# Optimization experiments

Hardware: AMD Instinct MI355X
Metric: run time of the kernel (lower is better)

The kernel has to match this reference:

```python
import jax, jax.numpy as jnp
import numpy as np

N = 50000
E = 800000
IN_C = 128
HID = 8
OUT_C = 32
HEADS = (4, 4, 4)
NEG_SLOPE = 0.2


def gat_conv(x, src, dst, W, att_src, att_dst, bias, heads, out_c, concat):
    # x: [N, F_in]; W: [F_in, heads*out_c]; att_*: [heads, out_c]; bias: [heads*out_c] or [out_c]
    n = x.shape[0]
    h = (x @ W).reshape(n, heads, out_c)                      # [N, H, C]
    a_src = (h * att_src).sum(-1)                             # [N, H]
    a_dst = (h * att_dst).sum(-1)                             # [N, H]
    e = jax.nn.leaky_relu(a_src[src] + a_dst[dst], NEG_SLOPE)  # [E, H]
    # segment softmax over edges grouped by destination node
    m = jax.ops.segment_max(e, dst, num_segments=n)           # [N, H]
    m = jnp.where(jnp.isfinite(m), m, 0.0)
    p = jnp.exp(e - m[dst])                                   # [E, H]
    s = jax.ops.segment_sum(p, dst, num_segments=n)           # [N, H]
    alpha = p / (s[dst] + 1e-16)                              # [E, H]
    msg = h[src] * alpha[:, :, None]                          # [E, H, C]
    out = jax.ops.segment_sum(msg, dst, num_segments=n)       # [N, H, C]
    out = out.reshape(n, heads * out_c) if concat else out.mean(axis=1)
    return out + bias


def setup_inputs() -> dict:
    key = jax.random.key(0)
    ks = jax.random.split(key, 16)
    x = jax.random.normal(ks[0], (N, IN_C), dtype=jnp.float32)
    edge_index = jax.random.randint(ks[1], (2, E), 0, N, dtype=jnp.int64)
    c1 = HID                       # per-head out of conv1 (8)
    c2 = HID * HEADS[0]            # per-head out of conv2 (32)
    c3 = OUT_C                     # per-head out of conv3 (32)
    in2 = HID * HEADS[0]           # 32
    in3 = HID * HEADS[0] * HEADS[1]  # 128
    sc = 0.1
    return {
        "x": x,
        "edge_index": edge_index,
        "W1": jax.random.normal(ks[2], (IN_C, HEADS[0] * c1), dtype=jnp.float32) * sc,
        "as1": jax.random.normal(ks[3], (HEADS[0], c1), dtype=jnp.float32) * sc,
        "ad1": jax.random.normal(ks[4], (HEADS[0], c1), dtype=jnp.float32) * sc,
        "b1": jnp.zeros((HEADS[0] * c1,), dtype=jnp.float32),
        "W2": jax.random.normal(ks[5], (in2, HEADS[1] * c2), dtype=jnp.float32) * sc,
        "as2": jax.random.normal(ks[6], (HEADS[1], c2), dtype=jnp.float32) * sc,
        "ad2": jax.random.normal(ks[7], (HEADS[1], c2), dtype=jnp.float32) * sc,
        "b2": jnp.zeros((HEADS[1] * c2,), dtype=jnp.float32),
        "W3": jax.random.normal(ks[8], (in3, HEADS[2] * c3), dtype=jnp.float32) * sc,
        "as3": jax.random.normal(ks[9], (HEADS[2], c3), dtype=jnp.float32) * sc,
        "ad3": jax.random.normal(ks[10], (HEADS[2], c3), dtype=jnp.float32) * sc,
        "b3": jnp.zeros((c3,), dtype=jnp.float32),
    }


def reference(x, edge_index, W1, as1, ad1, b1, W2, as2, ad2, b2, W3, as3, ad3, b3):
    src, dst = edge_index[0], edge_index[1]
    h = gat_conv(x, src, dst, W1, as1, ad1, b1, HEADS[0], HID, True)
    h = jax.nn.elu(h)
    h = gat_conv(h, src, dst, W2, as2, ad2, b2, HEADS[1], HID * HEADS[0], True)
    h = jax.nn.elu(h)
    out = gat_conv(h, src, dst, W3, as3, ad3, b3, HEADS[2], OUT_C, False)
    return out
```

## Files before the change

### kernel.cpp

```cpp
#include <hip/hip_runtime.h>
#include <hip/hip_fp16.h>

#define NEG_SLOPE 0.2f

static inline int cdiv(long long a, long long b) { return (int)((a + b - 1) / b); }

typedef _Float16 f16x8 __attribute__((ext_vector_type(8)));
typedef float f32x4 __attribute__((ext_vector_type(4)));

union h4u {
    float2  f2;
    __half2 h2[2];
};

__device__ __forceinline__ void load_sd(const void* ei_raw, int is64, int e, int E_,
                                        int& s, int& d)
{
    if (is64) {
        const long long* p = (const long long*)ei_raw;
        s = (int)p[e];
        d = (int)p[E_ + e];
    } else {
        const int* p = (const int*)ei_raw;
        s = p[e];
        d = p[E_ + e];
    }
}

__global__ __launch_bounds__(256) void prep_kernel(
    const void* __restrict__ ei, int E_, int n, int* __restrict__ flag,
    int* __restrict__ deg,
    const float* __restrict__ W1, __half* __restrict__ Wt1,
    const float* __restrict__ W2, __half* __restrict__ Wt2,
    const float* __restrict__ W3, __half* __restrict__ Wt3)
{
    int idx = blockIdx.x * 256 + threadIdx.x;

    if (blockIdx.x == 0) {
        __shared__ int bad;
        if (threadIdx.x == 0) bad = 0;
        __syncthreads();
        const long long* e64 = (const long long*)ei;
        int cnt = E_ < 512 ? E_ : 512;
        bool ok = true;
        for (int i = threadIdx.x; i < cnt; i += 256) {
            long long v = e64[i];
            if (v < 0 || v >= n) ok = false;
        }
        if (!ok) atomicAdd(&bad, 1);
        __syncthreads();
        if (threadIdx.x == 0) *flag = (bad == 0) ? 1 : 0;
    }

    if (idx < n) deg[idx] = 0;

    if (idx < 128 * 32) {
        int k = idx / 32, c = idx % 32;
        Wt1[c * 128 + k] = __float2half(W1[idx]);
    }
    if (idx < 32 * 128) {
        int k = idx / 128, c = idx % 128;
        Wt2[c * 32 + k] = __float2half(W2[idx]);
    }
    if (idx < 128 * 128) {
        int k = idx / 128, c = idx % 128;
        Wt3[c * 128 + k] = __float2half(W3[idx]);
    }
}

__global__ __launch_bounds__(256) void hist_kernel(const void* __restrict__ ei_raw,
                                                   const int* __restrict__ flag,
                                                   int* __restrict__ deg,
                                                   unsigned short* __restrict__ s16,
                                                   unsigned short* __restrict__ d16,
                                                   unsigned short* __restrict__ r16,
                                                   int E_)
{
    int base = blockIdx.x * 1024 + threadIdx.x;
    int is64 = *flag;
    int sj[4], dj[4], rj[4];
    bool v[4];
#pragma unroll
    for (int j = 0; j < 4; j++) {
        int e = base + j * 256;
        v[j] = e < E_;
        if (v[j]) load_sd(ei_raw, is64, e, E_, sj[j], dj[j]);
    }
#pragma unroll
    for (int j = 0; j < 4; j++) {
        int e = base + j * 256;
        if (v[j]) {
            s16[e] = (unsigned short)sj[j];
            d16[e] = (unsigned short)dj[j];
        }
    }
#pragma unroll
    for (int j = 0; j < 4; j++) {
        if (v[j]) rj[j] = atomicAdd(deg + dj[j], 1);
    }
#pragma unroll
    for (int j = 0; j < 4; j++) {
        int e = base + j * 256;
        if (v[j]) r16[e] = (unsigned short)rj[j];
    }
}

__device__ __forceinline__ int wave_incl_scan(int v)
{
    int lane = threadIdx.x & 63;
#pragma unroll
    for (int off = 1; off < 64; off <<= 1) {
        int t = __shfl_up(v, off);
        if (lane >= off) v += t;
    }
    return v;
}

__global__ __launch_bounds__(1024) void scan_part_kernel(const int* __restrict__ deg,
                                                         int* __restrict__ start,
                                                         int* __restrict__ bsum, int n)
{
    __shared__ int wsum[16];
    int i = blockIdx.x * 1024 + threadIdx.x;
    int wid = threadIdx.x >> 6, lane = threadIdx.x & 63;
    int v = (i < n) ? deg[i] : 0;
    int incl = wave_incl_scan(v);
    if (lane == 63) wsum[wid] = incl;
    __syncthreads();
    if (wid == 0) {
        int w = (lane < 16) ? wsum[lane] : 0;
        w = wave_incl_scan(w);
        if (lane < 16) wsum[lane] = w;
    }
    __syncthreads();
    int excl = incl - v + (wid ? wsum[wid - 1] : 0);
    if (i < n) start[i] = excl;
    if (threadIdx.x == 1023) bsum[blockIdx.x] = wsum[15];
}

__global__ __launch_bounds__(1024) void scan_add_kernel(const int* __restrict__ deg,
                                                        const int* __restrict__ bsum,
                                                        int* __restrict__ start, int n)
{
    __shared__ int off_sh;
    if (threadIdx.x == 0) {
        int s = 0;
        for (int j = 0; j < blockIdx.x; j++) s += bsum[j];
        off_sh = s;
    }
    __syncthreads();
    int i = blockIdx.x * 1024 + threadIdx.x;
    if (i >= n) return;
    int v = start[i] + off_sh;
    start[i] = v;
    if (i == n - 1) start[n] = v + deg[i];
}

__global__ __launch_bounds__(256) void scatter_kernel(
    const unsigned short* __restrict__ s16, const unsigned short* __restrict__ d16,
    const unsigned short* __restrict__ r16, const int* __restrict__ start,
    unsigned short* __restrict__ sorted_src, int E_)
{
    int base = blockIdx.x * 1024 + threadIdx.x;
    int sj[4], dj[4], rj[4];
    bool v[4];
#pragma unroll
    for (int j = 0; j < 4; j++) {
        int e = base + j * 256;
        v[j] = e < E_;
        sj[j] = v[j] ? (int)s16[e] : 0;
        dj[j] = v[j] ? (int)d16[e] : 0;
        rj[j] = v[j] ? (int)r16[e] : 0;
    }
    int pj[4];
#pragma unroll
    for (int j = 0; j < 4; j++) {
        if (v[j]) pj[j] = start[dj[j]] + rj[j];
    }
#pragma unroll
    for (int j = 0; j < 4; j++) {
        if (v[j])
            __builtin_nontemporal_store((unsigned short)sj[j], sorted_src + pj[j]);
    }
}

template <int K, int NOUT, int A16>
__global__ __launch_bounds__(256) void gemm_mfma_kernel(
    const void* __restrict__ xin, const __half* __restrict__ Wt,
    const float* __restrict__ att_s, const float* __restrict__ att_d,
    __half* __restrict__ h, float* __restrict__ a_s, float* __restrict__ a_d, int n)
{
    constexpr int KC = 32;
    constexpr int NT = NOUT / 16;
    constexpr int XP = KC + 8;
    constexpr int HP = NOUT + 8;
    constexpr int C  = NOUT / 4;

    __shared__ _Float16 Xs[64 * XP];
    __shared__ _Float16 Ws[NOUT * XP];
    __shared__ _Float16 Hs[64 * HP];
    __shared__ float As[NOUT], Ad[NOUT];

    const int tid  = threadIdx.x;
    const int nb   = blockIdx.x * 64;
    const int wave = tid >> 6, lane = tid & 63;
    const int m16  = lane & 15, quad = lane >> 4;

    if (tid < NOUT) { As[tid] = att_s[tid]; Ad[tid] = att_d[tid]; }

    f32x4 acc[NT];
#pragma unroll
    for (int t = 0; t < NT; t++) acc[t] = (f32x4){0.f, 0.f, 0.f, 0.f};

    for (int kc = 0; kc < K; kc += KC) {
        {
            int node = tid >> 2, seg = tid & 3;
            int gn = nb + node;
            f16x8 v = {0, 0, 0, 0, 0, 0, 0, 0};
            if (gn < n) {
                if (A16) {
                    v = *(const f16x8*)((const __half*)xin + (size_t)gn * K + kc +
                                        seg * 8);
                } else {
                    const float4* p =
                        (const float4*)((const float*)xin + (size_t)gn * K + kc + seg * 8);
                    float4 a = p[0], b = p[1];
                    v = (f16x8){(_Float16)a.x, (_Float16)a.y, (_Float16)a.z,
                                (_Float16)a.w, (_Float16)b.x, (_Float16)b.y,
                                (_Float16)b.z, (_Float16)b.w};
                }
            }
            *(f16x8*)&Xs[node * XP + seg * 8] = v;
        }
        for (int u = tid; u < NOUT * 4; u += 256) {
            int col = u >> 2, seg = u & 3;
            *(f16x8*)&Ws[col * XP + seg * 8] =
                *(const f16x8*)(Wt + (size_t)col * K + kc + seg * 8);
        }
        __syncthreads();

        f16x8 a = *(const f16x8*)&Xs[(wave * 16 + m16) * XP + quad * 8];
#pragma unroll
        for (int t = 0; t < NT; t++) {
            f16x8 b = *(const f16x8*)&Ws[(t * 16 + m16) * XP + quad * 8];
            acc[t] = __builtin_amdgcn_mfma_f32_16x16x32_f16(a, b, acc[t], 0, 0, 0);
        }
        __syncthreads();
    }

#pragma unroll
    for (int t = 0; t < NT; t++) {
#pragma unroll
        for (int r = 0; r < 4; r++) {
            int row = wave * 16 + quad * 4 + r;
            Hs[row * HP + t * 16 + m16] = (_Float16)acc[t][r];
        }
    }
    __syncthreads();

    for (int u = tid; u < 64 * NOUT / 8; u += 256) {
        int row = u / (NOUT / 8), seg = u % (NOUT / 8);
        int gn = nb + row;
        if (gn < n)
            *(f16x8*)(h + (size_t)gn * NOUT + seg * 8) =
                *(const f16x8*)&Hs[row * HP + seg * 8];
    }

    {
        int node = tid >> 2, head = tid & 3;
        int gn = nb + node;
        const _Float16* hr = &Hs[node * HP + head * C];
        float s1 = 0.f, s2 = 0.f;
#pragma unroll 4
        for (int c = 0; c < C; c++) {
            float v = (float)hr[c];
            s1 += v * As[head * C + c];
            s2 += v * Ad[head * C + c];
        }
        if (gn < n) {
            a_s[gn * 4 + head] = s1;
            a_d[gn * 4 + head] = s2;
        }
    }
}

template <int MODE>
__global__ __launch_bounds__(256) void gat_agg128_kernel(
    const int* __restrict__ start, const unsigned short* __restrict__ ss,
    const __half* __restrict__ h, const float* __restrict__ a_s,
    const float* __restrict__ a_d, const float* __restrict__ bias,
    void* __restrict__ out, int n)
{
    int local = threadIdx.x >> 5;
    int q     = threadIdx.x & 31;
    int node  = blockIdx.x * 8 + local;
    bool active = node < n;
    int s0 = 0, s1 = 0;
    if (active) { s0 = start[node]; s1 = start[node + 1]; }
    int head = q >> 3;
    float adh = active ? a_d[node * 4 + head] : 0.f;
    const float2* __restrict__ h2 = (const float2*)h + q;

    float4 acc = make_float4(0.f, 0.f, 0.f, 0.f);
    float sm = 0.f;
    int i = s0;
    for (; i + 8 <= s1; i += 8) {
        int    sj[8];
        float  ej[8];
        float2 rj[8];
#pragma unroll
        for (int j = 0; j < 8; j++) sj[j] = (int)ss[i + j];
#pragma unroll
        for (int j = 0; j < 8; j++) ej[j] = a_s[sj[j] * 4 + head];
#pragma unroll
        for (int j = 0; j < 8; j++) rj[j] = h2[(size_t)sj[j] * 32];
#pragma unroll
        for (int j = 0; j < 8; j++) {
            float e = ej[j] + adh;
            e = e > 0.f ? e : NEG_SLOPE * e;
            float p = __expf(e);
            sm += p;
            h4u u; u.f2 = rj[j];
            float2 lo = __half22float2(u.h2[0]);
            float2 hi = __half22float2(u.h2[1]);
            acc.x += lo.x * p; acc.y += lo.y * p;
            acc.z += hi.x * p; acc.w += hi.y * p;
        }
    }
    for (; i < s1; i++) {
        int s = (int)ss[i];
        float e = a_s[s * 4 + head] + adh;
        e = e > 0.f ? e : NEG_SLOPE * e;
        float p = __expf(e);
        sm += p;
        h4u u; u.f2 = h2[(size_t)s * 32];
        float2 lo = __half22float2(u.h2[0]);
        float2 hi = __half22float2(u.h2[1]);
        acc.x += lo.x * p; acc.y += lo.y * p;
        acc.z += hi.x * p; acc.w += hi.y * p;
    }

    float inv = 1.f / (sm + 1e-16f);
    acc.x *= inv; acc.y *= inv; acc.z *= inv; acc.w *= inv;

    if (MODE == 0) {
        if (active) {
            float4 b4 = ((const float4*)bias)[q];
            float4 v = make_float4(acc.x + b4.x, acc.y + b4.y, acc.z + b4.z,
                                   acc.w + b4.w);
            v.x = v.x > 0.f ? v.x : (__expf(v.x) - 1.f);
            v.y = v.y > 0.f ? v.y : (__expf(v.y) - 1.f);
            v.z = v.z > 0.f ? v.z : (__expf(v.z) - 1.f);
            v.w = v.w > 0.f ? v.w : (__expf(v.w) - 1.f);
            h4u u;
            u.h2[0] = __floats2half2_rn(v.x, v.y);
            u.h2[1] = __floats2half2_rn(v.z, v.w);
            *(float2*)((__half*)out + (size_t)node * 128 + q * 4) = u.f2;
        }
    } else {
        __shared__ float4 sh4[8][33];
        sh4[local][q] = acc;
        __syncthreads();
        if (q < 8 && active) {
            float4 a = sh4[local][q];
            float4 b = sh4[local][q + 8];
            float4 c = sh4[local][q + 16];
            float4 d = sh4[local][q + 24];
            float4 b4 = ((const float4*)bias)[q];
            float4 r = make_float4(0.25f * (a.x + b.x + c.x + d.x) + b4.x,
                                   0.25f * (a.y + b.y + c.y + d.y) + b4.y,
                                   0.25f * (a.z + b.z + c.z + d.z) + b4.z,
                                   0.25f * (a.w + b.w + c.w + d.w) + b4.w);
            *(float4*)((float*)out + (size_t)node * 32 + q * 4) = r;
        }
    }
}

__global__ __launch_bounds__(256) void gat_agg32_kernel(
    const int* __restrict__ start, const unsigned short* __restrict__ ss,
    const __half* __restrict__ h, const float* __restrict__ a_s,
    const float* __restrict__ a_d, const float* __restrict__ bias,
    __half* __restrict__ out, int n)
{
    int local = threadIdx.x >> 3;
    int q     = threadIdx.x & 7;
    int node  = blockIdx.x * 32 + local;
    bool active = node < n;
    int s0 = 0, s1 = 0;
    if (active) { s0 = start[node]; s1 = start[node + 1]; }
    int head = q >> 1;
    float adh = active ? a_d[node * 4 + head] : 0.f;
    const float2* __restrict__ h2 = (const float2*)h + q;

    float4 acc = make_float4(0.f, 0.f, 0.f, 0.f);
    float sm = 0.f;
    int i = s0;
    for (; i + 8 <= s1; i += 8) {
        int    sj[8];
        float  ej[8];
        float2 rj[8];
#pragma unroll
        for (int j = 0; j < 8; j++) sj[j] = (int)ss[i + j];
#pragma unroll
        for (int j = 0; j < 8; j++) ej[j] = a_s[sj[j] * 4 + head];
#pragma unroll
        for (int j = 0; j < 8; j++) rj[j] = h2[(size_t)sj[j] * 8];
#pragma unroll
        for (int j = 0; j < 8; j++) {
            float e = ej[j] + adh;
            e = e > 0.f ? e : NEG_SLOPE * e;
            float p = __expf(e);
            sm += p;
            h4u u; u.f2 = rj[j];
            float2 lo = __half22float2(u.h2[0]);
            float2 hi = __half22float2(u.h2[1]);
            acc.x += lo.x * p; acc.y += lo.y * p;
            acc.z += hi.x * p; acc.w += hi.y * p;
        }
    }
    for (; i < s1; i++) {
        int s = (int)ss[i];
        float e = a_s[s * 4 + head] + adh;
        e = e > 0.f ? e : NEG_SLOPE * e;
        float p = __expf(e);
        sm += p;
        h4u u; u.f2 = h2[(size_t)s * 8];
        float2 lo = __half22float2(u.h2[0]);
        float2 hi = __half22float2(u.h2[1]);
        acc.x += lo.x * p; acc.y += lo.y * p;
        acc.z += hi.x * p; acc.w += hi.y * p;
    }

    if (active) {
        float inv = 1.f / (sm + 1e-16f);
        float4 b4 = ((const float4*)bias)[q];
        float4 v = make_float4(acc.x * inv + b4.x, acc.y * inv + b4.y,
                               acc.z * inv + b4.z, acc.w * inv + b4.w);
        v.x = v.x > 0.f ? v.x : (__expf(v.x) - 1.f);
        v.y = v.y > 0.f ? v.y : (__expf(v.y) - 1.f);
        v.z = v.z > 0.f ? v.z : (__expf(v.z) - 1.f);
        v.w = v.w > 0.f ? v.w : (__expf(v.w) - 1.f);
        h4u u;
        u.h2[0] = __floats2half2_rn(v.x, v.y);
        u.h2[1] = __floats2half2_rn(v.z, v.w);
        *(float2*)(out + (size_t)node * 32 + q * 4) = u.f2;
    }
}


extern "C" void kernel_launch(void* const* d_in, const int* in_sizes, int n_in,
                              void* d_out, int out_size, void* d_ws, size_t ws_size,
                              hipStream_t stream)
{
    const float* x   = (const float*)d_in[0];
    const void*  ei  = d_in[1];
    const float* W1  = (const float*)d_in[2];
    const float* as1 = (const float*)d_in[3];
    const float* ad1 = (const float*)d_in[4];
    const float* b1  = (const float*)d_in[5];
    const float* W2  = (const float*)d_in[6];
    const float* as2 = (const float*)d_in[7];
    const float* ad2 = (const float*)d_in[8];
    const float* b2  = (const float*)d_in[9];
    const float* W3  = (const float*)d_in[10];
    const float* as3 = (const float*)d_in[11];
    const float* ad3 = (const float*)d_in[12];
    const float* b3  = (const float*)d_in[13];
    float* out = (float*)d_out;

    const int N_ = in_sizes[0] / 128;
    const int E_ = in_sizes[1] / 2;

    char* ws = (char*)d_ws;
    size_t off = 0;
    auto alloc = [&](size_t nbytes) -> void* {
        void* p = ws + off;
        off += (nbytes + 255) & ~(size_t)255;
        return p;
    };
    __half* h          = (__half*)alloc((size_t)N_ * 128 * 2);
    __half* x2h        = (__half*)alloc((size_t)N_ * 32 * 2);
    __half* x3h        = (__half*)alloc((size_t)N_ * 128 * 2);
    __half* Wt1        = (__half*)alloc(128 * 32 * 2);
    __half* Wt2        = (__half*)alloc(32 * 128 * 2);
    __half* Wt3        = (__half*)alloc(128 * 128 * 2);
    float* asrc        = (float*)alloc((size_t)N_ * 4 * 4);
    float* adst        = (float*)alloc((size_t)N_ * 4 * 4);
    int*   deg         = (int*)alloc((size_t)N_ * 4);
    int*   start       = (int*)alloc((size_t)(N_ + 1) * 4);
    unsigned short* sorted_src = (unsigned short*)alloc((size_t)E_ * 2);
    unsigned short* s16        = (unsigned short*)alloc((size_t)E_ * 2);
    unsigned short* d16        = (unsigned short*)alloc((size_t)E_ * 2);
    unsigned short* r16        = (unsigned short*)alloc((size_t)E_ * 2);
    int*   bsum        = (int*)alloc(4096);
    int*   flag        = (int*)alloc(256);

    const int gN8  = cdiv(N_, 8);
    const int gN32 = cdiv(N_, 32);
    const int gN64 = cdiv(N_, 64);
    const int nSB  = cdiv(N_, 1024);
    int prepWork = N_ > 128 * 128 ? N_ : 128 * 128;

    prep_kernel<<<cdiv(prepWork, 256), 256, 0, stream>>>(ei, E_, N_, flag, deg,
                                                         W1, Wt1, W2, Wt2, W3, Wt3);
    hist_kernel<<<cdiv(E_, 1024), 256, 0, stream>>>(ei, flag, deg, s16, d16, r16, E_);
    scan_part_kernel<<<nSB, 1024, 0, stream>>>(deg, start, bsum, N_);
    scan_add_kernel<<<nSB, 1024, 0, stream>>>(deg, bsum, start, N_);
    scatter_kernel<<<cdiv(E_, 1024), 256, 0, stream>>>(s16, d16, r16, start,
                                                       sorted_src, E_);

    gemm_mfma_kernel<128, 32, 0><<<gN64, 256, 0, stream>>>(x, Wt1, as1, ad1, h,
                                                           asrc, adst, N_);
    gat_agg32_kernel<<<gN32, 256, 0, stream>>>(start, sorted_src, h, asrc, adst, b1,
                                               x2h, N_);

    gemm_mfma_kernel<32, 128, 1><<<gN64, 256, 0, stream>>>(x2h, Wt2, as2, ad2, h,
                                                           asrc, adst, N_);
    gat_agg128_kernel<0><<<gN8, 256, 0, stream>>>(start, sorted_src, h, asrc, adst, b2,
                                                  x3h, N_);

    gemm_mfma_kernel<128, 128, 1><<<gN64, 256, 0, stream>>>(x3h, Wt3, as3, ad3, h,
                                                            asrc, adst, N_);
    gat_agg128_kernel<1><<<gN8, 256, 0, stream>>>(start, sorted_src, h, asrc, adst, b3,
                                                  out, N_);
}
```

Measured before the change: 285.9 us.

## Fuse CSR build into one cooperative kernel and deepen aggregation unroll

```diff
diff --git a/kernel.cpp b/kernel.cpp
--- a/kernel.cpp
+++ b/kernel.cpp
@@ -1,5 +1,8 @@
 #include <hip/hip_runtime.h>
 #include <hip/hip_fp16.h>
+#include <hip/hip_cooperative_groups.h>
+
+namespace cg = cooperative_groups;
 
 #define NEG_SLOPE 0.2f
 
@@ -27,19 +30,51 @@
     }
 }
 
-__global__ __launch_bounds__(256) void prep_kernel(
-    const void* __restrict__ ei, int E_, int n, int* __restrict__ flag,
+__device__ __forceinline__ int wave_incl_scan(int v)
+{
+    int lane = threadIdx.x & 63;
+#pragma unroll
+    for (int off = 1; off < 64; off <<= 1) {
+        int t = __shfl_up(v, off);
+        if (lane >= off) v += t;
+    }
+    return v;
+}
+
+__global__ __launch_bounds__(256) void csr_kernel(
+    const void* __restrict__ ei, int E_, int n,
     int* __restrict__ deg,
+    unsigned short* __restrict__ s16, unsigned short* __restrict__ d16,
+    unsigned short* __restrict__ r16,
+    int* __restrict__ start, int* __restrict__ bsum,
+    unsigned short* __restrict__ sorted_src,
     const float* __restrict__ W1, __half* __restrict__ Wt1,
     const float* __restrict__ W2, __half* __restrict__ Wt2,
     const float* __restrict__ W3, __half* __restrict__ Wt3)
 {
-    int idx = blockIdx.x * 256 + threadIdx.x;
-
-    if (blockIdx.x == 0) {
-        __shared__ int bad;
-        if (threadIdx.x == 0) bad = 0;
-        __syncthreads();
+    cg::grid_group grid = cg::this_grid();
+    const int nB    = gridDim.x;
+    const int gsize = nB * 256;
+    const int gtid  = blockIdx.x * 256 + threadIdx.x;
+
+    for (int i = gtid; i < n; i += gsize) deg[i] = 0;
+    for (int i = gtid; i < 128 * 32; i += gsize) {
+        int k = i / 32, c = i % 32;
+        Wt1[c * 128 + k] = __float2half(W1[i]);
+    }
+    for (int i = gtid; i < 32 * 128; i += gsize) {
+        int k = i / 128, c = i % 128;
+        Wt2[c * 32 + k] = __float2half(W2[i]);
+    }
+    for (int i = gtid; i < 128 * 128; i += gsize) {
+        int k = i / 128, c = i % 128;
+        Wt3[c * 128 + k] = __float2half(W3[i]);
+    }
+
+    __shared__ int bad_sh;
+    if (threadIdx.x == 0) bad_sh = 0;
+    __syncthreads();
+    {
         const long long* e64 = (const long long*)ei;
         int cnt = E_ < 512 ? E_ : 512;
         bool ok = true;
@@ -47,140 +82,108 @@
             long long v = e64[i];
             if (v < 0 || v >= n) ok = false;
         }
-        if (!ok) atomicAdd(&bad, 1);
-        __syncthreads();
-        if (threadIdx.x == 0) *flag = (bad == 0) ? 1 : 0;
-    }
-
-    if (idx < n) deg[idx] = 0;
-
-    if (idx < 128 * 32) {
-        int k = idx / 32, c = idx % 32;
-        Wt1[c * 128 + k] = __float2half(W1[idx]);
-    }
-    if (idx < 32 * 128) {
-        int k = idx / 128, c = idx % 128;
-        Wt2[c * 32 + k] = __float2half(W2[idx]);
-    }
-    if (idx < 128 * 128) {
-        int k = idx / 128, c = idx % 128;
-        Wt3[c * 128 + k] = __float2half(W3[idx]);
-    }
-}
-
-__global__ __launch_bounds__(256) void hist_kernel(const void* __restrict__ ei_raw,
-                                                   const int* __restrict__ flag,
-                                                   int* __restrict__ deg,
-                                                   unsigned short* __restrict__ s16,
-                                                   unsigned short* __restrict__ d16,
-                                                   unsigned short* __restrict__ r16,
-                                                   int E_)
-{
-    int base = blockIdx.x * 1024 + threadIdx.x;
-    int is64 = *flag;
-    int sj[4], dj[4], rj[4];
-    bool v[4];
-#pragma unroll
-    for (int j = 0; j < 4; j++) {
-        int e = base + j * 256;
-        v[j] = e < E_;
-        if (v[j]) load_sd(ei_raw, is64, e, E_, sj[j], dj[j]);
-    }
-#pragma unroll
-    for (int j = 0; j < 4; j++) {
-        int e = base + j * 256;
-        if (v[j]) {
-            s16[e] = (unsigned short)sj[j];
-            d16[e] = (unsigned short)dj[j];
-        }
-    }
-#pragma unroll
-    for (int j = 0; j < 4; j++) {
-        if (v[j]) rj[j] = atomicAdd(deg + dj[j], 1);
-    }
-#pragma unroll
-    for (int j = 0; j < 4; j++) {
-        int e = base + j * 256;
-        if (v[j]) r16[e] = (unsigned short)rj[j];
-    }
-}
-
-__device__ __forceinline__ int wave_incl_scan(int v)
-{
-    int lane = threadIdx.x & 63;
-#pragma unroll
-    for (int off = 1; off < 64; off <<= 1) {
-        int t = __shfl_up(v, off);
-        if (lane >= off) v += t;
-    }
-    return v;
-}
-
-__global__ __launch_bounds__(1024) void scan_part_kernel(const int* __restrict__ deg,
-                                                         int* __restrict__ start,
-                                                         int* __restrict__ bsum, int n)
-{
-    __shared__ int wsum[16];
-    int i = blockIdx.x * 1024 + threadIdx.x;
-    int wid = threadIdx.x >> 6, lane = threadIdx.x & 63;
-    int v = (i < n) ? deg[i] : 0;
-    int incl = wave_incl_scan(v);
-    if (lane == 63) wsum[wid] = incl;
+        if (!ok) atomicAdd(&bad_sh, 1);
+    }
     __syncthreads();
-    if (wid == 0) {
-        int w = (lane < 16) ? wsum[lane] : 0;
-        w = wave_incl_scan(w);
-        if (lane < 16) wsum[lane] = w;
-    }
+    const int is64 = (bad_sh == 0);
+
+    grid.sync();
+
+    for (int base = blockIdx.x * 1024 + threadIdx.x; base < E_; base += gsize * 4) {
+        int sj[4], dj[4], rj[4];
+        bool v[4];
+#pragma unroll
+        for (int j = 0; j < 4; j++) {
+            int e = base + j * 256;
+            v[j] = e < E_;
+            if (v[j]) load_sd(ei, is64, e, E_, sj[j], dj[j]);
+        }
+#pragma unroll
+        for (int j = 0; j < 4; j++) {
+            int e = base + j * 256;
+            if (v[j]) {
+                s16[e] = (unsigned short)sj[j];
+                d16[e] = (unsigned short)dj[j];
+            }
+        }
+#pragma unroll
+        for (int j = 0; j < 4; j++) {
+            if (v[j]) rj[j] = atomicAdd(deg + dj[j], 1);
+        }
+#pragma unroll
+        for (int j = 0; j < 4; j++) {
+            int e = base + j * 256;
+            if (v[j]) r16[e] = (unsigned short)rj[j];
+        }
+    }
+
+    grid.sync();
+
+    const int C  = (n + nB - 1) / nB;
+    const int c0 = blockIdx.x * C;
+    const int c1 = (c0 + C) < n ? (c0 + C) : n;
+    __shared__ int wsum[4];
+    __shared__ int carry_sh;
+    if (threadIdx.x == 0) carry_sh = 0;
     __syncthreads();
-    int excl = incl - v + (wid ? wsum[wid - 1] : 0);
-    if (i < n) start[i] = excl;
-    if (threadIdx.x == 1023) bsum[blockIdx.x] = wsum[15];
-}
-
-__global__ __launch_bounds__(1024) void scan_add_kernel(const int* __restrict__ deg,
-                                                        const int* __restrict__ bsum,
-                                                        int* __restrict__ start, int n)
-{
-    __shared__ int off_sh;
-    if (threadIdx.x == 0) {
-        int s = 0;
-        for (int j = 0; j < blockIdx.x; j++) s += bsum[j];
-        off_sh = s;
-    }
-    __syncthreads();
-    int i = blockIdx.x * 1024 + threadIdx.x;
-    if (i >= n) return;
-    int v = start[i] + off_sh;
-    start[i] = v;
-    if (i == n - 1) start[n] = v + deg[i];
-}
-
-__global__ __launch_bounds__(256) void scatter_kernel(
-    const unsigned short* __restrict__ s16, const unsigned short* __restrict__ d16,
-    const unsigned short* __restrict__ r16, const int* __restrict__ start,
-    unsigned short* __restrict__ sorted_src, int E_)
-{
-    int base = blockIdx.x * 1024 + threadIdx.x;
-    int sj[4], dj[4], rj[4];
-    bool v[4];
-#pragma unroll
-    for (int j = 0; j < 4; j++) {
-        int e = base + j * 256;
-        v[j] = e < E_;
-        sj[j] = v[j] ? (int)s16[e] : 0;
-        dj[j] = v[j] ? (int)d16[e] : 0;
-        rj[j] = v[j] ? (int)r16[e] : 0;
-    }
-    int pj[4];
-#pragma unroll
-    for (int j = 0; j < 4; j++) {
-        if (v[j]) pj[j] = start[dj[j]] + rj[j];
-    }
-#pragma unroll
-    for (int j = 0; j < 4; j++) {
-        if (v[j])
-            __builtin_nontemporal_store((unsigned short)sj[j], sorted_src + pj[j]);
+    for (int t = c0; t < c1; t += 256) {
+        int i = t + threadIdx.x;
+        int v = (i < c1) ? deg[i] : 0;
+        int incl = wave_incl_scan(v);
+        int wid = threadIdx.x >> 6, lane = threadIdx.x & 63;
+        if (lane == 63) wsum[wid] = incl;
+        __syncthreads();
+        int woff = 0;
+        for (int w = 0; w < wid; w++) woff += wsum[w];
+        int carry = carry_sh;
+        int excl = incl - v + woff + carry;
+        if (i < c1) start[i] = excl;
+        __syncthreads();
+        if (threadIdx.x == 255) carry_sh = carry + woff + incl;
+        __syncthreads();
+    }
+    if (threadIdx.x == 0) bsum[blockIdx.x] = carry_sh;
+
+    grid.sync();
+
+    __shared__ int red[256];
+    {
+        int partial = 0;
+        for (int j = threadIdx.x; j < blockIdx.x; j += 256) partial += bsum[j];
+        red[threadIdx.x] = partial;
+        __syncthreads();
+        for (int s = 128; s > 0; s >>= 1) {
+            if (threadIdx.x < s) red[threadIdx.x] += red[threadIdx.x + s];
+            __syncthreads();
+        }
+    }
+    int off0 = red[0];
+    for (int i = c0 + threadIdx.x; i < c1; i += 256) start[i] += off0;
+    if (blockIdx.x == 0 && threadIdx.x == 0) start[n] = E_;
+
+    grid.sync();
+
+    for (int base = blockIdx.x * 1024 + threadIdx.x; base < E_; base += gsize * 4) {
+        int sj[4], dj[4], rj[4];
+        bool v[4];
+#pragma unroll
+        for (int j = 0; j < 4; j++) {
+            int e = base + j * 256;
+            v[j] = e < E_;
+            sj[j] = v[j] ? (int)s16[e] : 0;
+            dj[j] = v[j] ? (int)d16[e] : 0;
+            rj[j] = v[j] ? (int)r16[e] : 0;
+        }
+        int pj[4];
+#pragma unroll
+        for (int j = 0; j < 4; j++) {
+            if (v[j]) pj[j] = start[dj[j]] + rj[j];
+        }
+#pragma unroll
+        for (int j = 0; j < 4; j++) {
+            if (v[j])
+                __builtin_nontemporal_store((unsigned short)sj[j], sorted_src + pj[j]);
+        }
     }
 }
 
@@ -304,18 +307,41 @@
     float4 acc = make_float4(0.f, 0.f, 0.f, 0.f);
     float sm = 0.f;
     int i = s0;
-    for (; i + 8 <= s1; i += 8) {
-        int    sj[8];
-        float  ej[8];
-        float2 rj[8];
-#pragma unroll
-        for (int j = 0; j < 8; j++) sj[j] = (int)ss[i + j];
-#pragma unroll
-        for (int j = 0; j < 8; j++) ej[j] = a_s[sj[j] * 4 + head];
-#pragma unroll
-        for (int j = 0; j < 8; j++) rj[j] = h2[(size_t)sj[j] * 32];
-#pragma unroll
-        for (int j = 0; j < 8; j++) {
+    for (; i + 16 <= s1; i += 16) {
+        int    sj[16];
+        float  ej[16];
+        float2 rj[16];
+#pragma unroll
+        for (int j = 0; j < 16; j++) sj[j] = (int)ss[i + j];
+#pragma unroll
+        for (int j = 0; j < 16; j++) ej[j] = a_s[sj[j] * 4 + head];
+#pragma unroll
+        for (int j = 0; j < 16; j++) rj[j] = h2[(size_t)sj[j] * 32];
+#pragma unroll
+        for (int j = 0; j < 16; j++) {
+            float e = ej[j] + adh;
+            e = e > 0.f ? e : NEG_SLOPE * e;
+            float p = __expf(e);
+            sm += p;
+            h4u u; u.f2 = rj[j];
+            float2 lo = __half22float2(u.h2[0]);
+            float2 hi = __half22float2(u.h2[1]);
+            acc.x += lo.x * p; acc.y += lo.y * p;
+            acc.z += hi.x * p; acc.w += hi.y * p;
+        }
+    }
+    for (; i + 4 <= s1; i += 4) {
+        int    sj[4];
+        float  ej[4];
+        float2 rj[4];
+#pragma unroll
+        for (int j = 0; j < 4; j++) sj[j] = (int)ss[i + j];
+#pragma unroll
+        for (int j = 0; j < 4; j++) ej[j] = a_s[sj[j] * 4 + head];
+#pragma unroll
+        for (int j = 0; j < 4; j++) rj[j] = h2[(size_t)sj[j] * 32];
+#pragma unroll
+        for (int j = 0; j < 4; j++) {
             float e = ej[j] + adh;
             e = e > 0.f ? e : NEG_SLOPE * e;
             float p = __expf(e);
@@ -395,18 +421,41 @@
     float4 acc = make_float4(0.f, 0.f, 0.f, 0.f);
     float sm = 0.f;
     int i = s0;
-    for (; i + 8 <= s1; i += 8) {
-        int    sj[8];
-        float  ej[8];
-        float2 rj[8];
-#pragma unroll
-        for (int j = 0; j < 8; j++) sj[j] = (int)ss[i + j];
-#pragma unroll
-        for (int j = 0; j < 8; j++) ej[j] = a_s[sj[j] * 4 + head];
-#pragma unroll
-        for (int j = 0; j < 8; j++) rj[j] = h2[(size_t)sj[j] * 8];
-#pragma unroll
-        for (int j = 0; j < 8; j++) {
+    for (; i + 16 <= s1; i += 16) {
+        int    sj[16];
+        float  ej[16];
+        float2 rj[16];
+#pragma unroll
+        for (int j = 0; j < 16; j++) sj[j] = (int)ss[i + j];
+#pragma unroll
+        for (int j = 0; j < 16; j++) ej[j] = a_s[sj[j] * 4 + head];
+#pragma unroll
+        for (int j = 0; j < 16; j++) rj[j] = h2[(size_t)sj[j] * 8];
+#pragma unroll
+        for (int j = 0; j < 16; j++) {
+            float e = ej[j] + adh;
+            e = e > 0.f ? e : NEG_SLOPE * e;
+            float p = __expf(e);
+            sm += p;
+            h4u u; u.f2 = rj[j];
+            float2 lo = __half22float2(u.h2[0]);
+            float2 hi = __half22float2(u.h2[1]);
+            acc.x += lo.x * p; acc.y += lo.y * p;
+            acc.z += hi.x * p; acc.w += hi.y * p;
+        }
+    }
+    for (; i + 4 <= s1; i += 4) {
+        int    sj[4];
+        float  ej[4];
+        float2 rj[4];
+#pragma unroll
+        for (int j = 0; j < 4; j++) sj[j] = (int)ss[i + j];
+#pragma unroll
+        for (int j = 0; j < 4; j++) ej[j] = a_s[sj[j] * 4 + head];
+#pragma unroll
+        for (int j = 0; j < 4; j++) rj[j] = h2[(size_t)sj[j] * 8];
+#pragma unroll
+        for (int j = 0; j < 4; j++) {
             float e = ej[j] + adh;
             e = e > 0.f ? e : NEG_SLOPE * e;
             float p = __expf(e);
@@ -493,21 +542,21 @@
     unsigned short* d16        = (unsigned short*)alloc((size_t)E_ * 2);
     unsigned short* r16        = (unsigned short*)alloc((size_t)E_ * 2);
     int*   bsum        = (int*)alloc(4096);
-    int*   flag        = (int*)alloc(256);
 
     const int gN8  = cdiv(N_, 8);
     const int gN32 = cdiv(N_, 32);
     const int gN64 = cdiv(N_, 64);
-    const int nSB  = cdiv(N_, 1024);
-    int prepWork = N_ > 128 * 128 ? N_ : 128 * 128;
-
-    prep_kernel<<<cdiv(prepWork, 256), 256, 0, stream>>>(ei, E_, N_, flag, deg,
-                                                         W1, Wt1, W2, Wt2, W3, Wt3);
-    hist_kernel<<<cdiv(E_, 1024), 256, 0, stream>>>(ei, flag, deg, s16, d16, r16, E_);
-    scan_part_kernel<<<nSB, 1024, 0, stream>>>(deg, start, bsum, N_);
-    scan_add_kernel<<<nSB, 1024, 0, stream>>>(deg, bsum, start, N_);
-    scatter_kernel<<<cdiv(E_, 1024), 256, 0, stream>>>(s16, d16, r16, start,
-                                                       sorted_src, E_);
+
+    {
+        int nCsrB = 784;
+        void* cargs[] = {(void*)&ei,  (void*)&E_,  (void*)&N_,   (void*)&deg,
+                         (void*)&s16, (void*)&d16, (void*)&r16,  (void*)&start,
+                         (void*)&bsum, (void*)&sorted_src,
+                         (void*)&W1,  (void*)&Wt1, (void*)&W2,   (void*)&Wt2,
+                         (void*)&W3,  (void*)&Wt3};
+        hipLaunchCooperativeKernel((void*)csr_kernel, dim3(nCsrB), dim3(256),
+                                   cargs, 0, stream);
+    }
 
     gemm_mfma_kernel<128, 32, 0><<<gN64, 256, 0, stream>>>(x, Wt1, as1, ad1, h,
                                                            asrc, adst, N_);
```

Result: slower. 590.6 us (+106.5%).
